# Performance work log

Hardware: AMD Instinct MI355X
Metric: run time of the kernel (lower is better)

## Reference

```python
import jax, jax.numpy as jnp
import numpy as np

B, T, HID = 2, 2048, 2048
N_HEADS, N_KV, HEAD_DIM = 32, 8, 64
THETA = 10000.0
SCALE = HEAD_DIM ** -0.5
STEPS = 2  # entries already in cache before this call (step_idx)


def _rope_cos_sin(pos):
    # pos: [B, T] int -> cos/sin [B, T, HEAD_DIM]
    inv_freq = 1.0 / (THETA ** (jnp.arange(0, HEAD_DIM, 2, dtype=jnp.float32) / HEAD_DIM))
    freqs = pos.astype(jnp.float32)[..., None] * inv_freq  # [B,T,D/2]
    emb = jnp.concatenate([freqs, freqs], axis=-1)
    return jnp.cos(emb), jnp.sin(emb)


def _rotate_half(x):
    x1, x2 = jnp.split(x, 2, axis=-1)
    return jnp.concatenate([-x2, x1], axis=-1)


def setup_inputs() -> dict:
    key = jax.random.key(0)
    ks = jax.random.split(key, 8)
    combined_states = jax.random.normal(ks[0], (B, T, 2 * HID), dtype=jnp.float32)
    # additive causal mask: 0 on/below diagonal, large negative above
    causal = jnp.tril(jnp.ones((T, T), dtype=bool))
    attention_mask = jnp.where(causal, 0.0, -1e9).astype(jnp.float32)[None, None].repeat(B, axis=0)
    position_ids = jnp.broadcast_to(jnp.arange(T, dtype=jnp.int32), (B, T))
    prev_k = jax.random.normal(ks[1], (STEPS, B, N_HEADS, T, HEAD_DIM), dtype=jnp.float32)
    prev_v = jax.random.normal(ks[2], (STEPS, B, N_HEADS, T, HEAD_DIM), dtype=jnp.float32)
    Wq = 0.02 * jax.random.normal(ks[3], (2 * HID, N_HEADS * HEAD_DIM), dtype=jnp.float32)
    Wk = 0.02 * jax.random.normal(ks[4], (2 * HID, N_KV * HEAD_DIM), dtype=jnp.float32)
    Wv = 0.02 * jax.random.normal(ks[5], (2 * HID, N_KV * HEAD_DIM), dtype=jnp.float32)
    Wo = 0.02 * jax.random.normal(ks[6], (N_HEADS * HEAD_DIM, HID), dtype=jnp.float32)
    return {"combined_states": combined_states, "attention_mask": attention_mask,
            "position_ids": position_ids, "prev_k": prev_k, "prev_v": prev_v,
            "Wq": Wq, "Wk": Wk, "Wv": Wv, "Wo": Wo}


def reference(combined_states, attention_mask, position_ids, prev_k, prev_v, Wq, Wk, Wv, Wo):
    b, t, _ = combined_states.shape
    step_idx = prev_k.shape[0]  # len(cache_k) before append
    groups = N_HEADS // N_KV

    # fused QKV projection -> [B, H, T, D]
    q = (combined_states @ Wq).reshape(b, t, N_HEADS, HEAD_DIM).transpose(0, 2, 1, 3)
    k = (combined_states @ Wk).reshape(b, t, N_KV, HEAD_DIM).transpose(0, 2, 1, 3)
    v = (combined_states @ Wv).reshape(b, t, N_KV, HEAD_DIM).transpose(0, 2, 1, 3)

    # RoPE with phase shift by step_idx
    cos, sin = _rope_cos_sin(position_ids + step_idx)
    cos, sin = cos[:, None], sin[:, None]  # [B,1,T,D]
    q = q * cos + _rotate_half(q) * sin
    k = k * cos + _rotate_half(k) * sin

    # GQA expansion (repeat_interleave over head dim)
    k = jnp.repeat(k, groups, axis=1)
    v = jnp.repeat(v, groups, axis=1)

    # cache after append: [prev_0, prev_1, ..., k_new]; k0 = cache[0], later = cache[1:]
    k0, v0 = prev_k[0], prev_v[0]
    later_k = jnp.concatenate([prev_k[1:], k[None]], axis=0)  # [S, B, H, T, D], S = step_idx
    later_v = jnp.concatenate([prev_v[1:], v[None]], axis=0)

    # block attention over K_0 plus growing diagonal terms
    attn = jnp.einsum('bhtd,bhsd->bhts', q, k0) * SCALE + attention_mask  # [B,H,T,T]
    diag = jnp.einsum('bhtd,sbhtd->bhts', q, later_k) * SCALE             # [B,H,T,S]
    logits = jnp.concatenate([attn, diag], axis=-1)                        # [B,H,T,T+S]
    probs = jax.nn.softmax(logits.astype(jnp.float32), axis=-1).astype(q.dtype)

    out = jnp.einsum('bhts,bhsd->bhtd', probs[..., :t], v0)
    out = out + jnp.einsum('bhts,sbhtd->bhtd', probs[..., t:], later_v)
    out = out.transpose(0, 2, 1, 3).reshape(b, t, N_HEADS * HEAD_DIM)
    return out @ Wo
```

## Files before the change

kernel.cpp:

```cpp
#include <hip/hip_runtime.h>

#define B_    2
#define T_    2048
#define HID_  2048
#define NH_   32
#define NKV_  8
#define HD_   64
#define STEPS_ 2
#define SCALE_ 0.125f
#define CSC_  0.18033688011112042f

typedef float   f32x4  __attribute__((ext_vector_type(4)));
typedef __bf16  bf16x8 __attribute__((ext_vector_type(8)));
typedef unsigned short u16x8 __attribute__((ext_vector_type(8)));

__device__ __forceinline__ unsigned short f2bf(float f) {
  unsigned int u = __builtin_bit_cast(unsigned int, f);
  u = (u + 0x7fffu + ((u >> 16) & 1u)) >> 16;
  return (unsigned short)u;
}
__device__ __forceinline__ float bf2f(unsigned short h) {
  unsigned int u = ((unsigned int)h) << 16;
  return __builtin_bit_cast(float, u);
}
__device__ __forceinline__ bf16x8 frag_ld(const unsigned short* p) {
  u16x8 v = *(const u16x8*)p;
  return __builtin_bit_cast(bf16x8, v);
}
__device__ __forceinline__ f32x4 mfma16(bf16x8 a, bf16x8 b, f32x4 c) {
  return __builtin_amdgcn_mfma_f32_16x16x32_bf16(a, b, c, 0, 0, 0);
}
__device__ __forceinline__ void async_cp16(const void* g, void* l) {
  __builtin_amdgcn_global_load_lds(
      (const __attribute__((address_space(1))) void*)g,
      (__attribute__((address_space(3))) void*)l, 16, 0, 0);
}
__device__ __forceinline__ unsigned int cvtpk_bf16(float lo, float hi) {
  unsigned int r;
  asm("v_cvt_pk_bf16_f32 %0, %1, %2" : "=v"(r) : "v"(lo), "v"(hi));
  return r;
}

__global__ __launch_bounds__(256) void convert_bf16(const float* __restrict__ in,
                                                    unsigned short* __restrict__ out,
                                                    int n4) {
  int idx = blockIdx.x * 256 + threadIdx.x;
  if (idx < n4) {
    float4 v = ((const float4*)in)[idx];
    ushort4 o;
    o.x = f2bf(v.x); o.y = f2bf(v.y); o.z = f2bf(v.z); o.w = f2bf(v.w);
    ((ushort4*)out)[idx] = o;
  }
}

__global__ __launch_bounds__(256) void transpose_f32_bf16_ld(const float* __restrict__ in,
                                                             unsigned short* __restrict__ out,
                                                             int K, int N, int ldo) {
  __shared__ float tile[64][65];
  int n0 = blockIdx.x * 64, k0 = blockIdx.y * 64;
  int c = threadIdx.x & 63, w = threadIdx.x >> 6;
#pragma unroll
  for (int i = 0; i < 16; i++) {
    int r = w * 16 + i;
    tile[r][c] = in[(size_t)(k0 + r) * N + n0 + c];
  }
  __syncthreads();
#pragma unroll
  for (int i = 0; i < 16; i++) {
    int rr = w * 16 + i;
    out[(size_t)(n0 + rr) * ldo + k0 + c] = f2bf(tile[c][rr]);
  }
}

__global__ __launch_bounds__(256) void transpose_v0(const float* __restrict__ v0,
                                                    unsigned short* __restrict__ v0t) {
  __shared__ float tile[64][65];
  int s0 = blockIdx.x * 64;
  int bh = blockIdx.y;
  const float* src = v0 + (size_t)bh * T_ * HD_;
  unsigned short* dst = v0t + (size_t)bh * HD_ * T_;
  int c = threadIdx.x & 63, w = threadIdx.x >> 6;
#pragma unroll
  for (int i = 0; i < 16; i++) {
    int r = w * 16 + i;
    tile[r][c] = src[(size_t)(s0 + r) * HD_ + c];
  }
  __syncthreads();
#pragma unroll
  for (int i = 0; i < 16; i++) {
    int rr = w * 16 + i;
    dst[(size_t)rr * T_ + s0 + c] = f2bf(tile[c][rr]);
  }
}

#define SBAR  do { __builtin_amdgcn_sched_barrier(0); __builtin_amdgcn_s_barrier(); \
                   __builtin_amdgcn_sched_barrier(0); } while (0)
#define LGKM0 do { asm volatile("s_waitcnt lgkmcnt(0)" ::: "memory"); \
                   __builtin_amdgcn_sched_barrier(0); } while (0)
#define LGKM8 do { asm volatile("s_waitcnt lgkmcnt(8)" ::: "memory"); } while (0)
#define VM4   do { asm volatile("s_waitcnt vmcnt(4)" ::: "memory"); } while (0)
#define VM0   do { asm volatile("s_waitcnt vmcnt(0)" ::: "memory"); } while (0)

__global__ __launch_bounds__(512, 2) void gemm256_bt(const unsigned short* __restrict__ A,
                                                     const unsigned short* __restrict__ Bt,
                                                     float* __restrict__ C,
                                                     int M, int N, int K) {
  __shared__ __attribute__((aligned(128))) unsigned short smem[2][4][8192];

  const int tid  = threadIdx.x;
  const int lane = tid & 63;
  const int wid  = tid >> 6;
  const int wr   = wid >> 2;
  const int wc   = wid & 3;
  const int la   = lane & 15;
  const int lq   = lane >> 4;
  const int sw   = la & 7;
  const int m0   = blockIdx.x * 256;
  const int n0   = blockIdx.y * 256;

  const int sr = lane >> 3;
  const int sl = (lane & 7) ^ sr;

  const unsigned short* gA[2][2];
  const unsigned short* gB[2][2];
#pragma unroll
  for (int h = 0; h < 2; ++h)
#pragma unroll
    for (int is = 0; is < 2; ++is) {
      int r = (wid * 2 + is) * 8 + sr;
      gA[h][is] = A  + (size_t)(m0 + h * 128 + r) * K + sl * 8;
      gB[h][is] = Bt + (size_t)(n0 + h * 128 + r) * K + sl * 8;
    }

#define STG_A(buf, h, kt) do { \
    async_cp16(gA[h][0] + (kt) * 64, &smem[buf][h][(wid * 2 + 0) * 512]); \
    async_cp16(gA[h][1] + (kt) * 64, &smem[buf][h][(wid * 2 + 1) * 512]); \
  } while (0)
#define STG_B(buf, h, kt) do { \
    async_cp16(gB[h][0] + (kt) * 64, &smem[buf][2 + (h)][(wid * 2 + 0) * 512]); \
    async_cp16(gB[h][1] + (kt) * 64, &smem[buf][2 + (h)][(wid * 2 + 1) * 512]); \
  } while (0)

  f32x4  acc[8][4] = {};
  bf16x8 ar[8], b0r[4], b1r[4];

#define RD_A(buf, qm) do { \
    const unsigned short* rp_ = &smem[buf][wr][0]; \
    _Pragma("unroll") \
    for (int i_ = 0; i_ < 4; ++i_) { \
      int ro_ = ((qm) * 64 + i_ * 16 + la) * 64; \
      ar[i_ * 2 + 0] = frag_ld(rp_ + ro_ + (((0 + lq) ^ sw) << 3)); \
      ar[i_ * 2 + 1] = frag_ld(rp_ + ro_ + (((4 + lq) ^ sw) << 3)); \
    } \
  } while (0)
#define RD_B(buf, qn, breg) do { \
    const unsigned short* rp_ = &smem[buf][2 + (wc >> 1)][0]; \
    _Pragma("unroll") \
    for (int j_ = 0; j_ < 2; ++j_) { \
      int ro_ = ((wc & 1) * 64 + (qn) * 32 + j_ * 16 + la) * 64; \
      breg[j_ * 2 + 0] = frag_ld(rp_ + ro_ + (((0 + lq) ^ sw) << 3)); \
      breg[j_ * 2 + 1] = frag_ld(rp_ + ro_ + (((4 + lq) ^ sw) << 3)); \
    } \
  } while (0)
#define MMA_Q(qm, qn, breg) do { \
    _Pragma("unroll") \
    for (int i_ = 0; i_ < 4; ++i_) \
      _Pragma("unroll") \
      for (int j_ = 0; j_ < 2; ++j_) { \
        f32x4 c_ = acc[(qm) * 4 + i_][(qn) * 2 + j_]; \
        c_ = mfma16(ar[i_ * 2 + 0], breg[j_ * 2 + 0], c_); \
        c_ = mfma16(ar[i_ * 2 + 1], breg[j_ * 2 + 1], c_); \
        acc[(qm) * 4 + i_][(qn) * 2 + j_] = c_; \
      } \
  } while (0)

  STG_A(0, 0, 0); STG_A(0, 1, 0);
  STG_B(0, 0, 0); STG_B(0, 1, 0);
  STG_B(1, 0, 1); STG_B(1, 1, 1);
  VM4;
  SBAR;

  const int NI = K >> 7;
  for (int it = 0; it < NI; ++it) {
    const int e = it * 2;
    const bool pf = (it + 1 < NI);
    RD_A(0, 0);
    RD_B(0, 0, b0r);
    STG_A(1, 0, e + 1);
    LGKM8;
    SBAR; LGKM0;
    __builtin_amdgcn_s_setprio(1); MMA_Q(0, 0, b0r); __builtin_amdgcn_s_setprio(0);
    SBAR;
    RD_B(0, 1, b1r);
    STG_A(1, 1, e + 1);
    SBAR; LGKM0;
    __builtin_amdgcn_s_setprio(1); MMA_Q(0, 1, b1r); __builtin_amdgcn_s_setprio(0);
    SBAR;
    RD_A(0, 1);
    if (pf) STG_B(0, 0, e + 2);
    SBAR; LGKM0;
    __builtin_amdgcn_s_setprio(1); MMA_Q(1, 1, b1r); __builtin_amdgcn_s_setprio(0);
    SBAR;
    if (pf) STG_B(0, 1, e + 2);
    SBAR; LGKM0;
    __builtin_amdgcn_s_setprio(1); MMA_Q(1, 0, b0r); __builtin_amdgcn_s_setprio(0);
    if (pf) { VM4; } else { VM0; }
    SBAR;
    RD_A(1, 0);
    RD_B(1, 0, b0r);
    if (pf) STG_A(0, 0, e + 2);
    LGKM8;
    SBAR; LGKM0;
    __builtin_amdgcn_s_setprio(1); MMA_Q(0, 0, b0r); __builtin_amdgcn_s_setprio(0);
    SBAR;
    RD_B(1, 1, b1r);
    if (pf) STG_A(0, 1, e + 2);
    SBAR; LGKM0;
    __builtin_amdgcn_s_setprio(1); MMA_Q(0, 1, b1r); __builtin_amdgcn_s_setprio(0);
    SBAR;
    RD_A(1, 1);
    if (pf) STG_B(1, 0, e + 3);
    SBAR; LGKM0;
    __builtin_amdgcn_s_setprio(1); MMA_Q(1, 1, b1r); __builtin_amdgcn_s_setprio(0);
    SBAR;
    if (pf) STG_B(1, 1, e + 3);
    SBAR; LGKM0;
    __builtin_amdgcn_s_setprio(1); MMA_Q(1, 0, b0r); __builtin_amdgcn_s_setprio(0);
    VM4;
    SBAR;
  }

#pragma unroll
  for (int mf = 0; mf < 8; ++mf) {
    int row = m0 + wr * 128 + mf * 16 + lq * 4;
#pragma unroll
    for (int nf = 0; nf < 4; ++nf) {
      int col = n0 + wc * 64 + nf * 16 + la;
#pragma unroll
      for (int r = 0; r < 4; ++r)
        C[(size_t)(row + r) * N + col] = acc[mf][nf][r];
    }
  }
}

__global__ __launch_bounds__(256) void rope_kernel(const float* __restrict__ QKV,
                                                   const int* __restrict__ pos_ids,
                                                   unsigned short* __restrict__ q_b,
                                                   float* __restrict__ knew) {
  int idx = blockIdx.x * 256 + threadIdx.x;
  const int total = B_ * T_ * (NH_ + NKV_) * 32;
  if (idx >= total) return;
  int i = idx & 31;
  int tmp = idx >> 5;
  int hh = tmp % (NH_ + NKV_);
  int bt = tmp / (NH_ + NKV_);
  int t = bt & (T_ - 1);
  int b = bt >> 11;
  int pos = pos_ids[bt] + STEPS_;
  float inv = exp2f(-(float)i * (13.287712379549449f / 32.0f));
  float ang = (float)pos * inv;
  float sn, cs;
  sincosf(ang, &sn, &cs);
  const float* rowp = QKV + (size_t)bt * 3072;
  if (hh < NH_) {
    float x1 = rowp[hh * 64 + i];
    float x2 = rowp[hh * 64 + 32 + i];
    float y1 = (x1 * cs - x2 * sn) * CSC_;
    float y2 = (x2 * cs + x1 * sn) * CSC_;
    size_t o = ((size_t)(b * NH_ + hh) * T_ + t) * HD_ + i;
    q_b[o] = f2bf(y1);
    q_b[o + 32] = f2bf(y2);
  } else {
    int kv = hh - NH_;
    float x1 = rowp[2048 + kv * 64 + i];
    float x2 = rowp[2048 + kv * 64 + 32 + i];
    float y1 = x1 * cs - x2 * sn;
    float y2 = x2 * cs + x1 * sn;
    size_t o = ((size_t)(b * NKV_ + kv) * T_ + t) * HD_ + i;
    knew[o] = y1;
    knew[o + 32] = y2;
  }
}

__global__ __launch_bounds__(256, 3) void flash_kernel(const unsigned short* __restrict__ qb,
                                                       const unsigned short* __restrict__ k0b,
                                                       const unsigned short* __restrict__ v0t,
                                                       float* __restrict__ Of,
                                                       float* __restrict__ ml) {
  __shared__ unsigned short sK[2][64 * 64];
  __shared__ unsigned short sV[2][64 * 64];
  __shared__ unsigned short sP[4][16 * 72];

  const int tid = threadIdx.x;
  const int lane = tid & 63;
  const int wave = tid >> 6;
  const int la = lane & 15;
  const int lq = lane >> 4;
  const int swz = la & 7;

  const int id = blockIdx.x;
  const int bh = (id & 7) * 8 + ((id >> 3) & 7);
  const int qt = 15 - (id >> 6);

  const size_t bhs = (size_t)bh;
  const unsigned short* gK = k0b + bhs * T_ * HD_;
  const unsigned short* gV = v0t + bhs * HD_ * T_;

  const int rb0 = qt * 128 + wave * 32;
  const int ktd = rb0 >> 6;
  const int ktmax = 2 * qt + 1;

  bf16x8 aq[2][2];
#pragma unroll
  for (int f = 0; f < 2; f++) {
    const unsigned short* qp = qb + (bhs * T_ + rb0 + f * 16 + la) * HD_;
    aq[f][0] = frag_ld(qp + lq * 8);
    aq[f][1] = frag_ld(qp + 32 + lq * 8);
  }

  f32x4 o[2][4] = {};
  float m_f[2] = {-1e30f, -1e30f};
  float l_f[2] = {0.0f, 0.0f};

  const int lrow = lane >> 3;
  const int lcb = (lane & 7) ^ lrow;

  {
    unsigned short* kd = &sK[0][wave * 1024];
    unsigned short* vd = &sV[0][wave * 1024];
    async_cp16(gK + (size_t)(wave * 16 + lrow) * HD_ + lcb * 8, kd);
    async_cp16(gK + (size_t)(wave * 16 + 8 + lrow) * HD_ + lcb * 8, kd + 512);
    async_cp16(gV + (size_t)(wave * 16 + lrow) * T_ + lcb * 8, vd);
    async_cp16(gV + (size_t)(wave * 16 + 8 + lrow) * T_ + lcb * 8, vd + 512);
  }
  __syncthreads();

  int cur = 0;
  for (int kt = 0; kt <= ktmax; ++kt) {
    if (kt < ktmax) {
      const int nk = (kt + 1) * 64;
      unsigned short* kd = &sK[cur ^ 1][wave * 1024];
      unsigned short* vd = &sV[cur ^ 1][wave * 1024];
      async_cp16(gK + (size_t)(nk + wave * 16 + lrow) * HD_ + lcb * 8, kd);
      async_cp16(gK + (size_t)(nk + wave * 16 + 8 + lrow) * HD_ + lcb * 8, kd + 512);
      async_cp16(gV + (size_t)(wave * 16 + lrow) * T_ + nk + lcb * 8, vd);
      async_cp16(gV + (size_t)(wave * 16 + 8 + lrow) * T_ + nk + lcb * 8, vd + 512);
    }

    if (kt <= ktd) {
      const unsigned short* kb = &sK[cur][0];
      const unsigned short* vb = &sV[cur][0];

      bf16x8 bk0[4], bk1[4];
#pragma unroll
      for (int nb = 0; nb < 4; nb++) {
        const unsigned short* rp = kb + (nb * 16 + la) * 64;
        bk0[nb] = frag_ld(rp + ((lq ^ swz) << 3));
        bk1[nb] = frag_ld(rp + (((lq + 4) ^ swz) << 3));
      }
      f32x4 s[2][4];
      __builtin_amdgcn_s_setprio(1);
#pragma unroll
      for (int f = 0; f < 2; f++)
#pragma unroll
        for (int nb = 0; nb < 4; nb++) {
          f32x4 z = {0.f, 0.f, 0.f, 0.f};
          z = mfma16(bk0[nb], aq[f][0], z);
          z = mfma16(bk1[nb], aq[f][1], z);
          s[f][nb] = z;
        }
      __builtin_amdgcn_s_setprio(0);

      const bool diag = (kt == ktd);
#pragma unroll
      for (int f = 0; f < 2; f++) {
        const int qrow = rb0 + f * 16 + la;
        if (diag) {
#pragma unroll
          for (int nb = 0; nb < 4; nb++)
#pragma unroll
            for (int r = 0; r < 4; r++) {
              int key = kt * 64 + nb * 16 + lq * 4 + r;
              s[f][nb][r] = (key <= qrow) ? s[f][nb][r] : -1e30f;
            }
        }
        float t0 = fmaxf(fmaxf(s[f][0][0], s[f][0][1]), fmaxf(s[f][0][2], s[f][0][3]));
        float t1 = fmaxf(fmaxf(s[f][1][0], s[f][1][1]), fmaxf(s[f][1][2], s[f][1][3]));
        float t2 = fmaxf(fmaxf(s[f][2][0], s[f][2][1]), fmaxf(s[f][2][2], s[f][2][3]));
        float t3 = fmaxf(fmaxf(s[f][3][0], s[f][3][1]), fmaxf(s[f][3][2], s[f][3][3]));
        float tm = fmaxf(fmaxf(t0, t1), fmaxf(t2, t3));
        tm = fmaxf(tm, __shfl_xor(tm, 16));
        tm = fmaxf(tm, __shfl_xor(tm, 32));
        const bool resc = __any(tm > m_f[f] + 8.0f);
        if (resc) {
          float mn = fmaxf(m_f[f], tm);
          float al = exp2f(m_f[f] - mn);
          m_f[f] = mn;
          l_f[f] *= al;
          float a0 = __shfl(al, lq * 4 + 0);
          float a1 = __shfl(al, lq * 4 + 1);
          float a2 = __shfl(al, lq * 4 + 2);
          float a3 = __shfl(al, lq * 4 + 3);
#pragma unroll
          for (int jd = 0; jd < 4; jd++) {
            o[f][jd][0] *= a0;
            o[f][jd][1] *= a1;
            o[f][jd][2] *= a2;
            o[f][jd][3] *= a3;
          }
        }
        float ls = 0.0f;
#pragma unroll
        for (int nb = 0; nb < 4; nb++)
#pragma unroll
          for (int r = 0; r < 4; r++) {
            float p = exp2f(s[f][nb][r] - m_f[f]);
            s[f][nb][r] = p;
            ls += p;
          }
        ls += __shfl_xor(ls, 16);
        ls += __shfl_xor(ls, 32);
        l_f[f] += ls;
      }

      bf16x8 bv0[4], bv1[4];
#pragma unroll
      for (int jd = 0; jd < 4; jd++) {
        const unsigned short* rp = vb + (jd * 16 + la) * 64;
        bv0[jd] = frag_ld(rp + ((lq ^ swz) << 3));
        bv1[jd] = frag_ld(rp + (((lq + 4) ^ swz) << 3));
      }
      unsigned short* pw = &sP[wave][0];
#pragma unroll
      for (int f = 0; f < 2; f++) {
#pragma unroll
        for (int nb = 0; nb < 4; nb++) {
          unsigned int p01 = cvtpk_bf16(s[f][nb][0], s[f][nb][1]);
          unsigned int p23 = cvtpk_bf16(s[f][nb][2], s[f][nb][3]);
          unsigned long long pq = ((unsigned long long)p23 << 32) | (unsigned long long)p01;
          *(unsigned long long*)(pw + la * 72 + nb * 16 + lq * 4) = pq;
        }
        bf16x8 ap0 = frag_ld(&pw[la * 72 + lq * 8]);
        bf16x8 ap1 = frag_ld(&pw[la * 72 + 32 + lq * 8]);
        __builtin_amdgcn_s_setprio(1);
#pragma unroll
        for (int jd = 0; jd < 4; jd++) {
          o[f][jd] = mfma16(ap0, bv0[jd], o[f][jd]);
          o[f][jd] = mfma16(ap1, bv1[jd], o[f][jd]);
        }
        __builtin_amdgcn_s_setprio(0);
      }
    }
    __syncthreads();
    cur ^= 1;
  }

#pragma unroll
  for (int f = 0; f < 2; f++)
#pragma unroll
    for (int jd = 0; jd < 4; jd++)
#pragma unroll
      for (int r = 0; r < 4; r++) {
        int row = rb0 + f * 16 + lq * 4 + r;
        Of[(bhs * T_ + row) * HD_ + jd * 16 + la] = o[f][jd][r];
      }
  if (lq == 0) {
#pragma unroll
    for (int f = 0; f < 2; f++) {
      int row = rb0 + f * 16 + la;
      ml[(bhs * T_ + row) * 2] = m_f[f];
      ml[(bhs * T_ + row) * 2 + 1] = l_f[f];
    }
  }
}

__global__ __launch_bounds__(256) void attn_epilogue(const unsigned short* __restrict__ qb,
                                                     const float* __restrict__ prev_k,
                                                     const float* __restrict__ prev_v,
                                                     const float* __restrict__ knew,
                                                     const float* __restrict__ QKV,
                                                     const float* __restrict__ Of,
                                                     const float* __restrict__ ml,
                                                     unsigned short* __restrict__ attnout) {
  const int lane = threadIdx.x & 63;
  const int wave = threadIdx.x >> 6;
  const int row = blockIdx.x * 4 + wave;
  const int b = row >> 16;
  const int h = (row >> 11) & 31;
  const int t = row & 2047;
  const int d = lane;
  const size_t base = (size_t)row * HD_ + d;

  float q = bf2f(qb[base]);
  const size_t p1i = ((size_t)B_ * NH_ * T_ * HD_) + (((size_t)b * NH_ + h) * T_ + t) * HD_ + d;
  float k1 = prev_k[p1i];
  float v1 = prev_v[p1i];
  int kv = h >> 2;
  float kn = knew[(((size_t)b * NKV_ + kv) * T_ + t) * HD_ + d];
  float vn = QKV[((size_t)(b * T_ + t)) * 3072 + 2560 + kv * 64 + d];

  float e1 = q * k1, e2 = q * kn;
#pragma unroll
  for (int off = 1; off < 64; off <<= 1) {
    e1 += __shfl_xor(e1, off);
    e2 += __shfl_xor(e2, off);
  }

  float m = ml[(size_t)row * 2];
  float l = ml[(size_t)row * 2 + 1];
  float mf = fmaxf(m, fmaxf(e1, e2));
  float w0 = exp2f(m - mf), w1 = exp2f(e1 - mf), w2 = exp2f(e2 - mf);
  float denom = l * w0 + w1 + w2;
  float out = (Of[base] * w0 + v1 * w1 + vn * w2) / denom;

  attnout[((size_t)(b * T_ + t)) * (NH_ * HD_) + h * HD_ + d] = f2bf(out);
}

#define OFF_QKV   ((size_t)0)
#define OFF_XB    ((size_t)50331648)
#define OFF_WQKVT ((size_t)83886080)
#define OFF_WOT   ((size_t)109051904)
#define OFF_QB    ((size_t)117440512)
#define OFF_K0B   ((size_t)134217728)
#define OFF_V0T   ((size_t)150994944)
#define OFF_KNEW  ((size_t)167772160)
#define OFF_ML    ((size_t)176160768)

extern "C" void kernel_launch(void* const* d_in, const int* in_sizes, int n_in,
                              void* d_out, int out_size, void* d_ws, size_t ws_size,
                              hipStream_t stream) {
  const float* X = (const float*)d_in[0];
  const int* pos = (const int*)d_in[2];
  const float* prevk = (const float*)d_in[3];
  const float* prevv = (const float*)d_in[4];
  const float* Wq = (const float*)d_in[5];
  const float* Wk = (const float*)d_in[6];
  const float* Wv = (const float*)d_in[7];
  const float* Wo = (const float*)d_in[8];

  char* ws = (char*)d_ws;
  float* QKV = (float*)(ws + OFF_QKV);
  unsigned short* Xb = (unsigned short*)(ws + OFF_XB);
  float* Of = (float*)(ws + OFF_XB);
  unsigned short* WqkvT = (unsigned short*)(ws + OFF_WQKVT);
  unsigned short* attnout = (unsigned short*)(ws + OFF_WQKVT);
  unsigned short* WoT = (unsigned short*)(ws + OFF_WOT);
  unsigned short* q_b = (unsigned short*)(ws + OFF_QB);
  unsigned short* k0b = (unsigned short*)(ws + OFF_K0B);
  unsigned short* v0t = (unsigned short*)(ws + OFF_V0T);
  float* knew = (float*)(ws + OFF_KNEW);
  float* ml = (float*)(ws + OFF_ML);

  convert_bf16<<<16384, 256, 0, stream>>>(X, Xb, 4194304);
  transpose_f32_bf16_ld<<<dim3(32, 64), 256, 0, stream>>>(Wq, WqkvT, 4096, 2048, 4096);
  transpose_f32_bf16_ld<<<dim3(8, 64), 256, 0, stream>>>(Wk, WqkvT + (size_t)2048 * 4096, 4096, 512, 4096);
  transpose_f32_bf16_ld<<<dim3(8, 64), 256, 0, stream>>>(Wv, WqkvT + (size_t)2560 * 4096, 4096, 512, 4096);
  transpose_f32_bf16_ld<<<dim3(32, 32), 256, 0, stream>>>(Wo, WoT, 2048, 2048, 2048);
  convert_bf16<<<8192, 256, 0, stream>>>(prevk, k0b, 2097152);
  transpose_v0<<<dim3(32, 64), 256, 0, stream>>>(prevv, v0t);

  gemm256_bt<<<dim3(16, 12), 512, 0, stream>>>(Xb, WqkvT, QKV, 4096, 3072, 4096);

  rope_kernel<<<20480, 256, 0, stream>>>(QKV, pos, q_b, knew);

  flash_kernel<<<1024, 256, 0, stream>>>(q_b, k0b, v0t, Of, ml);

  attn_epilogue<<<32768, 256, 0, stream>>>(q_b, prevk, prevv, knew, QKV, Of, ml, attnout);

  gemm256_bt<<<dim3(16, 8), 512, 0, stream>>>(attnout, WoT, (float*)d_out, 4096, 2048, 2048);
}
```

Measured before the change: 556.1 us.

## Replace 256x256 GEMM tiles with templated 128xN tiles to fill more CUs

Replaces the 256x256-tile GEMM with a templated kernel using 128-row tiles and 384 or 256-column tiles. The QKV projection launches 256 workgroups instead of 192, and the output projection launches 256 instead of 128, which better fills the GPU's compute units. The staging and prefetch schedule is rebuilt to match the new tile shapes, with adjusted vmcnt waits. Smaller tiles reuse each loaded A and B row less, so global and LDS traffic per FLOP goes up.

```diff
diff --git a/kernel.cpp b/kernel.cpp
--- a/kernel.cpp
+++ b/kernel.cpp
@@ -97,15 +97,17 @@
                    __builtin_amdgcn_sched_barrier(0); } while (0)
 #define LGKM0 do { asm volatile("s_waitcnt lgkmcnt(0)" ::: "memory"); \
                    __builtin_amdgcn_sched_barrier(0); } while (0)
-#define LGKM8 do { asm volatile("s_waitcnt lgkmcnt(8)" ::: "memory"); } while (0)
-#define VM4   do { asm volatile("s_waitcnt vmcnt(4)" ::: "memory"); } while (0)
+#define VM2   do { asm volatile("s_waitcnt vmcnt(2)" ::: "memory"); } while (0)
 #define VM0   do { asm volatile("s_waitcnt vmcnt(0)" ::: "memory"); } while (0)
 
-__global__ __launch_bounds__(512, 2) void gemm256_bt(const unsigned short* __restrict__ A,
+template <int NF>
+__global__ __launch_bounds__(512, 2) void gemm128_bt(const unsigned short* __restrict__ A,
                                                      const unsigned short* __restrict__ Bt,
                                                      float* __restrict__ C,
                                                      int M, int N, int K) {
-  __shared__ __attribute__((aligned(128))) unsigned short smem[2][4][8192];
+  constexpr int NHF = NF / 2;
+  constexpr int BROWS = 128 + NF * 64;
+  __shared__ __attribute__((aligned(128))) unsigned short smem[2][BROWS * 64];
 
   const int tid  = threadIdx.x;
   const int lane = tid & 63;
@@ -115,132 +117,137 @@
   const int la   = lane & 15;
   const int lq   = lane >> 4;
   const int sw   = la & 7;
-  const int m0   = blockIdx.x * 256;
-  const int n0   = blockIdx.y * 256;
+  const int m0   = blockIdx.x * 128;
+  const int n0   = blockIdx.y * (NF * 64);
 
   const int sr = lane >> 3;
   const int sl = (lane & 7) ^ sr;
 
-  const unsigned short* gA[2][2];
-  const unsigned short* gB[2][2];
-#pragma unroll
-  for (int h = 0; h < 2; ++h)
-#pragma unroll
-    for (int is = 0; is < 2; ++is) {
-      int r = (wid * 2 + is) * 8 + sr;
-      gA[h][is] = A  + (size_t)(m0 + h * 128 + r) * K + sl * 8;
-      gB[h][is] = Bt + (size_t)(n0 + h * 128 + r) * K + sl * 8;
-    }
-
-#define STG_A(buf, h, kt) do { \
-    async_cp16(gA[h][0] + (kt) * 64, &smem[buf][h][(wid * 2 + 0) * 512]); \
-    async_cp16(gA[h][1] + (kt) * 64, &smem[buf][h][(wid * 2 + 1) * 512]); \
+  const unsigned short* gA[2];
+  const unsigned short* gB[NHF][2];
+#pragma unroll
+  for (int is = 0; is < 2; ++is) {
+    int r = (wid * 2 + is) * 8 + sr;
+    gA[is] = A + (size_t)(m0 + r) * K + sl * 8;
+#pragma unroll
+    for (int u = 0; u < NHF; ++u)
+      gB[u][is] = Bt + (size_t)(n0 + u * 128 + r) * K + sl * 8;
+  }
+
+#define G_STG_A(buf, kt) do { \
+    async_cp16(gA[0] + (size_t)(kt) * 64, &smem[buf][(wid * 2 + 0) * 512]); \
+    async_cp16(gA[1] + (size_t)(kt) * 64, &smem[buf][(wid * 2 + 1) * 512]); \
   } while (0)
-#define STG_B(buf, h, kt) do { \
-    async_cp16(gB[h][0] + (kt) * 64, &smem[buf][2 + (h)][(wid * 2 + 0) * 512]); \
-    async_cp16(gB[h][1] + (kt) * 64, &smem[buf][2 + (h)][(wid * 2 + 1) * 512]); \
+#define G_STG_B(buf, u, kt) do { \
+    async_cp16(gB[u][0] + (size_t)(kt) * 64, &smem[buf][(128 + (u) * 128) * 64 + (wid * 2 + 0) * 512]); \
+    async_cp16(gB[u][1] + (size_t)(kt) * 64, &smem[buf][(128 + (u) * 128) * 64 + (wid * 2 + 1) * 512]); \
   } while (0)
 
-  f32x4  acc[8][4] = {};
-  bf16x8 ar[8], b0r[4], b1r[4];
-
-#define RD_A(buf, qm) do { \
-    const unsigned short* rp_ = &smem[buf][wr][0]; \
+  f32x4  acc[4][NF] = {};
+  bf16x8 aR[2][2], b0r[NHF][2], b1r[NHF][2];
+
+#define G_RD_A(buf, qm) do { \
+    const unsigned short* rp_ = &smem[buf][0]; \
     _Pragma("unroll") \
-    for (int i_ = 0; i_ < 4; ++i_) { \
-      int ro_ = ((qm) * 64 + i_ * 16 + la) * 64; \
-      ar[i_ * 2 + 0] = frag_ld(rp_ + ro_ + (((0 + lq) ^ sw) << 3)); \
-      ar[i_ * 2 + 1] = frag_ld(rp_ + ro_ + (((4 + lq) ^ sw) << 3)); \
+    for (int i_ = 0; i_ < 2; ++i_) { \
+      int ro_ = (wr * 64 + (qm) * 32 + i_ * 16 + la) * 64; \
+      aR[i_][0] = frag_ld(rp_ + ro_ + (((0 + lq) ^ sw) << 3)); \
+      aR[i_][1] = frag_ld(rp_ + ro_ + (((4 + lq) ^ sw) << 3)); \
     } \
   } while (0)
-#define RD_B(buf, qn, breg) do { \
-    const unsigned short* rp_ = &smem[buf][2 + (wc >> 1)][0]; \
+#define G_RD_B(buf, qn, breg) do { \
+    const unsigned short* rp_ = &smem[buf][128 * 64]; \
     _Pragma("unroll") \
-    for (int j_ = 0; j_ < 2; ++j_) { \
-      int ro_ = ((wc & 1) * 64 + (qn) * 32 + j_ * 16 + la) * 64; \
-      breg[j_ * 2 + 0] = frag_ld(rp_ + ro_ + (((0 + lq) ^ sw) << 3)); \
-      breg[j_ * 2 + 1] = frag_ld(rp_ + ro_ + (((4 + lq) ^ sw) << 3)); \
+    for (int j_ = 0; j_ < NHF; ++j_) { \
+      int ro_ = (wc * (NF * 16) + (qn) * (NF * 8) + j_ * 16 + la) * 64; \
+      breg[j_][0] = frag_ld(rp_ + ro_ + (((0 + lq) ^ sw) << 3)); \
+      breg[j_][1] = frag_ld(rp_ + ro_ + (((4 + lq) ^ sw) << 3)); \
     } \
   } while (0)
-#define MMA_Q(qm, qn, breg) do { \
+#define G_MMA(qm, qn, breg) do { \
     _Pragma("unroll") \
-    for (int i_ = 0; i_ < 4; ++i_) \
+    for (int i_ = 0; i_ < 2; ++i_) \
       _Pragma("unroll") \
-      for (int j_ = 0; j_ < 2; ++j_) { \
-        f32x4 c_ = acc[(qm) * 4 + i_][(qn) * 2 + j_]; \
-        c_ = mfma16(ar[i_ * 2 + 0], breg[j_ * 2 + 0], c_); \
-        c_ = mfma16(ar[i_ * 2 + 1], breg[j_ * 2 + 1], c_); \
-        acc[(qm) * 4 + i_][(qn) * 2 + j_] = c_; \
+      for (int j_ = 0; j_ < NHF; ++j_) { \
+        f32x4 c_ = acc[(qm) * 2 + i_][(qn) * NHF + j_]; \
+        c_ = mfma16(aR[i_][0], breg[j_][0], c_); \
+        c_ = mfma16(aR[i_][1], breg[j_][1], c_); \
+        acc[(qm) * 2 + i_][(qn) * NHF + j_] = c_; \
       } \
   } while (0)
 
-  STG_A(0, 0, 0); STG_A(0, 1, 0);
-  STG_B(0, 0, 0); STG_B(0, 1, 0);
-  STG_B(1, 0, 1); STG_B(1, 1, 1);
-  VM4;
+  G_STG_A(0, 0);
+#pragma unroll
+  for (int u = 0; u < NHF; ++u) G_STG_B(0, u, 0);
+  if constexpr (NF == 6) G_STG_B(1, 2, 1); else G_STG_A(1, 1);
+  VM2;
   SBAR;
 
   const int NI = K >> 7;
   for (int it = 0; it < NI; ++it) {
     const int e = it * 2;
     const bool pf = (it + 1 < NI);
-    RD_A(0, 0);
-    RD_B(0, 0, b0r);
-    STG_A(1, 0, e + 1);
-    LGKM8;
-    SBAR; LGKM0;
-    __builtin_amdgcn_s_setprio(1); MMA_Q(0, 0, b0r); __builtin_amdgcn_s_setprio(0);
-    SBAR;
-    RD_B(0, 1, b1r);
-    STG_A(1, 1, e + 1);
-    SBAR; LGKM0;
-    __builtin_amdgcn_s_setprio(1); MMA_Q(0, 1, b1r); __builtin_amdgcn_s_setprio(0);
-    SBAR;
-    RD_A(0, 1);
-    if (pf) STG_B(0, 0, e + 2);
-    SBAR; LGKM0;
-    __builtin_amdgcn_s_setprio(1); MMA_Q(1, 1, b1r); __builtin_amdgcn_s_setprio(0);
-    SBAR;
-    if (pf) STG_B(0, 1, e + 2);
-    SBAR; LGKM0;
-    __builtin_amdgcn_s_setprio(1); MMA_Q(1, 0, b0r); __builtin_amdgcn_s_setprio(0);
-    if (pf) { VM4; } else { VM0; }
-    SBAR;
-    RD_A(1, 0);
-    RD_B(1, 0, b0r);
-    if (pf) STG_A(0, 0, e + 2);
-    LGKM8;
-    SBAR; LGKM0;
-    __builtin_amdgcn_s_setprio(1); MMA_Q(0, 0, b0r); __builtin_amdgcn_s_setprio(0);
-    SBAR;
-    RD_B(1, 1, b1r);
-    if (pf) STG_A(0, 1, e + 2);
-    SBAR; LGKM0;
-    __builtin_amdgcn_s_setprio(1); MMA_Q(0, 1, b1r); __builtin_amdgcn_s_setprio(0);
-    SBAR;
-    RD_A(1, 1);
-    if (pf) STG_B(1, 0, e + 3);
-    SBAR; LGKM0;
-    __builtin_amdgcn_s_setprio(1); MMA_Q(1, 1, b1r); __builtin_amdgcn_s_setprio(0);
-    SBAR;
-    if (pf) STG_B(1, 1, e + 3);
-    SBAR; LGKM0;
-    __builtin_amdgcn_s_setprio(1); MMA_Q(1, 0, b0r); __builtin_amdgcn_s_setprio(0);
-    VM4;
-    SBAR;
-  }
-
-#pragma unroll
-  for (int mf = 0; mf < 8; ++mf) {
-    int row = m0 + wr * 128 + mf * 16 + lq * 4;
-#pragma unroll
-    for (int nf = 0; nf < 4; ++nf) {
-      int col = n0 + wc * 64 + nf * 16 + la;
+    G_RD_A(0, 0);
+    G_RD_B(0, 0, b0r);
+    if constexpr (NF == 6) G_STG_A(1, e + 1); else G_STG_B(1, 0, e + 1);
+    SBAR; LGKM0;
+    __builtin_amdgcn_s_setprio(1); G_MMA(0, 0, b0r); __builtin_amdgcn_s_setprio(0);
+    SBAR;
+    G_RD_B(0, 1, b1r);
+    if constexpr (NF == 6) G_STG_B(1, 0, e + 1); else G_STG_B(1, 1, e + 1);
+    SBAR; LGKM0;
+    __builtin_amdgcn_s_setprio(1); G_MMA(0, 1, b1r); __builtin_amdgcn_s_setprio(0);
+    SBAR;
+    G_RD_A(0, 1);
+    if constexpr (NF == 6) G_STG_B(1, 1, e + 1);
+    SBAR; LGKM0;
+    __builtin_amdgcn_s_setprio(1); G_MMA(1, 1, b1r); __builtin_amdgcn_s_setprio(0);
+    SBAR;
+    if (pf) G_STG_A(0, e + 2);
+    SBAR; LGKM0;
+    __builtin_amdgcn_s_setprio(1); G_MMA(1, 0, b0r); __builtin_amdgcn_s_setprio(0);
+    if (pf) { VM2; } else { VM0; }
+    SBAR;
+    G_RD_A(1, 0);
+    G_RD_B(1, 0, b0r);
+    if (pf) G_STG_B(0, 0, e + 2);
+    SBAR; LGKM0;
+    __builtin_amdgcn_s_setprio(1); G_MMA(0, 0, b0r); __builtin_amdgcn_s_setprio(0);
+    SBAR;
+    G_RD_B(1, 1, b1r);
+    if (pf) G_STG_B(0, 1, e + 2);
+    SBAR; LGKM0;
+    __builtin_amdgcn_s_setprio(1); G_MMA(0, 1, b1r); __builtin_amdgcn_s_setprio(0);
+    SBAR;
+    G_RD_A(1, 1);
+    if constexpr (NF == 6) { if (pf) G_STG_B(0, 2, e + 2); }
+    SBAR; LGKM0;
+    __builtin_amdgcn_s_setprio(1); G_MMA(1, 1, b1r); __builtin_amdgcn_s_setprio(0);
+    SBAR;
+    if constexpr (NF == 6) { if (pf) G_STG_B(1, 2, e + 3); }
+    else                   { if (pf) G_STG_A(1, e + 3); }
+    SBAR; LGKM0;
+    __builtin_amdgcn_s_setprio(1); G_MMA(1, 0, b0r); __builtin_amdgcn_s_setprio(0);
+    VM2;
+    SBAR;
+  }
+
+#pragma unroll
+  for (int mf = 0; mf < 4; ++mf) {
+    int row = m0 + wr * 64 + mf * 16 + lq * 4;
+#pragma unroll
+    for (int nf = 0; nf < NF; ++nf) {
+      int col = n0 + wc * (NF * 16) + nf * 16 + la;
 #pragma unroll
       for (int r = 0; r < 4; ++r)
         C[(size_t)(row + r) * N + col] = acc[mf][nf][r];
     }
   }
+#undef G_STG_A
+#undef G_STG_B
+#undef G_RD_A
+#undef G_RD_B
+#undef G_MMA
 }
 
 __global__ __launch_bounds__(256) void rope_kernel(const float* __restrict__ QKV,
@@ -559,7 +566,7 @@
   convert_bf16<<<8192, 256, 0, stream>>>(prevk, k0b, 2097152);
   transpose_v0<<<dim3(32, 64), 256, 0, stream>>>(prevv, v0t);
 
-  gemm256_bt<<<dim3(16, 12), 512, 0, stream>>>(Xb, WqkvT, QKV, 4096, 3072, 4096);
+  gemm128_bt<6><<<dim3(32, 8), 512, 0, stream>>>(Xb, WqkvT, QKV, 4096, 3072, 4096);
 
   rope_kernel<<<20480, 256, 0, stream>>>(QKV, pos, q_b, knew);
 
@@ -567,5 +574,5 @@
 
   attn_epilogue<<<32768, 256, 0, stream>>>(q_b, prevk, prevv, knew, QKV, Of, ml, attnout);
 
-  gemm256_bt<<<dim3(16, 8), 512, 0, stream>>>(attnout, WoT, (float*)d_out, 4096, 2048, 2048);
-}
+  gemm128_bt<4><<<dim3(32, 8), 512, 0, stream>>>(attnout, WoT, (float*)d_out, 4096, 2048, 2048);
+}
```

New measurement: 523.1 us. 5.9% less time.
